# Performance work log

Hardware: AMD Instinct MI355X
Metric: run time of the kernel (lower is better)

Reference implementation:

```python
import jax, jax.numpy as jnp
import numpy as np

N_NODES = 50000
N_EDGES = 800000
D_IN = 128
D_OUT = 128
BN_EPS = 1e-5

# (component index, sign) per (column block j, row block i) of the octonion
# Hamilton matrix, matching make_octonion_mul's cat order exactly.
_OCT_TABLE = [
    [(0, 1), (1, -1), (2, -1), (3, -1), (4, -1), (5, -1), (6, -1), (7, -1)],
    [(1, 1), (0, 1), (3, -1), (2, 1), (5, -1), (4, 1), (7, 1), (6, -1)],
    [(2, 1), (3, 1), (0, 1), (1, -1), (6, -1), (7, -1), (4, 1), (5, 1)],
    [(3, 1), (2, -1), (1, 1), (0, 1), (7, -1), (6, 1), (5, -1), (4, 1)],
    [(4, 1), (5, 1), (6, 1), (7, 1), (0, 1), (1, -1), (2, -1), (3, -1)],
    [(5, 1), (4, -1), (7, 1), (6, -1), (1, 1), (0, 1), (3, 1), (2, -1)],
    [(6, 1), (7, -1), (4, -1), (5, 1), (2, 1), (3, -1), (0, 1), (1, 1)],
    [(7, 1), (6, 1), (5, -1), (4, -1), (3, 1), (2, 1), (1, -1), (0, 1)],
]


def make_octonion_mul(kernel):
    # kernel: [D_IN//8, D_OUT] -> hamilton: [D_IN, D_OUT]
    e = jnp.split(kernel, 8, axis=1)
    cols = [jnp.concatenate([s * e[i] for (i, s) in col], axis=0)
            for col in _OCT_TABLE]
    return jnp.concatenate(cols, axis=1)


def setup_inputs() -> dict:
    key = jax.random.key(0)
    k1, k2, k3, k4, k5 = jax.random.split(key, 5)
    stdv = np.sqrt(6.0 / (D_IN // 8 + D_OUT))
    return {
        "input": jax.random.normal(k1, (N_NODES, D_IN), dtype=jnp.float32),
        "adj_row": jax.random.randint(k2, (N_EDGES,), 0, N_NODES, dtype=jnp.int32),
        "adj_col": jax.random.randint(k3, (N_EDGES,), 0, N_NODES, dtype=jnp.int32),
        "adj_val": jax.random.uniform(k4, (N_EDGES,), dtype=jnp.float32),
        "weight": jax.random.uniform(k5, (D_IN // 8, D_OUT), dtype=jnp.float32,
                                     minval=-stdv, maxval=stdv),
        "gamma": jnp.ones((D_OUT,), dtype=jnp.float32),
        "beta": jnp.zeros((D_OUT,), dtype=jnp.float32),
    }


def reference(input, adj_row, adj_col, adj_val, weight, gamma, beta):
    hamilton = make_octonion_mul(weight)             # [D_IN, D_OUT]
    support = input @ hamilton                       # [N, D_OUT]
    # sparse adjacency spmm: out[r] += val * support[c]
    msg = adj_val[:, None] * support[adj_col]        # [E, D_OUT]
    out = jax.ops.segment_sum(msg, adj_row, num_segments=N_NODES)
    # BatchNorm1d (training mode: biased batch stats), then tanh
    mean = jnp.mean(out, axis=0)
    var = jnp.var(out, axis=0)
    normed = (out - mean) / jnp.sqrt(var + BN_EPS) * gamma + beta
    return jnp.tanh(normed)
```

## Files before the change

### kernel.cpp

```cpp
#include <hip/hip_runtime.h>
#include <hip/hip_fp16.h>
#include <math.h>

#define N_NODES 50000
#define N_EDGES 800000
#define D 128
#define BN_EPS 1e-5f
#define N_TILES 3125
#define CAP 48
#define SPMM_BLOCKS 2048
#define SCOLS 32
#define BINS 512
#define RPB 98
#define EPB 3125
#define SORTB 256
#define BCAP 2048
#define GEMMB 782

typedef __attribute__((ext_vector_type(8))) _Float16 half8;
typedef __attribute__((ext_vector_type(4))) float floatx4;

__device__ __constant__ int OCT_C[8][8] = {
    {0,1,2,3,4,5,6,7},
    {1,0,3,2,5,4,7,6},
    {2,3,0,1,6,7,4,5},
    {3,2,1,0,7,6,5,4},
    {4,5,6,7,0,1,2,3},
    {5,4,7,6,1,0,3,2},
    {6,7,4,5,2,3,0,1},
    {7,6,5,4,3,2,1,0}};
__device__ __constant__ float OCT_S[8][8] = {
    { 1,-1,-1,-1,-1,-1,-1,-1},
    { 1, 1,-1, 1,-1, 1, 1,-1},
    { 1, 1, 1,-1,-1,-1, 1, 1},
    { 1,-1, 1, 1,-1, 1,-1, 1},
    { 1, 1, 1, 1, 1,-1,-1,-1},
    { 1,-1, 1,-1, 1, 1, 1,-1},
    { 1,-1,-1, 1, 1,-1, 1, 1},
    { 1, 1,-1,-1, 1, 1,-1, 1}};

__global__ __launch_bounds__(256) void setup_kernel(const float* __restrict__ W,
                                                    __half* __restrict__ Ht,
                                                    float* __restrict__ stats,
                                                    int* __restrict__ bintail) {
    const int i = blockIdx.x * 256 + threadIdx.x;
    if (i < D * D) {
        int ccol = i >> 7, k = i & 127;
        int ii = k >> 4, kw = k & 15, j = ccol >> 4, m = ccol & 15;
        Ht[i] = __float2half(OCT_S[j][ii] * W[kw * D + OCT_C[j][ii] * 16 + m]);
    }
    if (i < 2 * D) stats[i] = 0.0f;
    if (i < BINS * 16) bintail[i] = 0;
}

__global__ __launch_bounds__(256) void sortgemm_kernel(const int* __restrict__ arow,
                                                       const int* __restrict__ acol,
                                                       const float* __restrict__ aval,
                                                       int* __restrict__ bintail,
                                                       uint2* __restrict__ binned,
                                                       const float* __restrict__ in,
                                                       const __half* __restrict__ Ht,
                                                       __half* __restrict__ support) {
    __shared__ uint2 stage[EPB];
    __shared__ int hist[BINS], pref[BINS], lbase[BINS], cursor[BINS];
    __shared__ int wtot[4];
    const int b = blockIdx.x;
    const int tid = threadIdx.x;
    if (b < SORTB) {
        const int lane = tid & 63, wid = tid >> 6;
        hist[tid] = 0; hist[tid + 256] = 0;
        __syncthreads();
        const int e0 = b * EPB, e1 = e0 + EPB;
        for (int i = e0 + tid; i < e1; i += 256)
            atomicAdd(&hist[arow[i] / RPB], 1);
        __syncthreads();
        int v0 = hist[2 * tid], v1 = hist[2 * tid + 1];
        int s = v0 + v1;
        int incl = s;
#pragma unroll
        for (int off = 1; off < 64; off <<= 1) {
            int t = __shfl_up(incl, off, 64);
            if (lane >= off) incl += t;
        }
        if (lane == 63) wtot[wid] = incl;
        __syncthreads();
        if (tid == 0) {
            int acc = 0;
#pragma unroll
            for (int w = 0; w < 4; ++w) { int t = wtot[w]; wtot[w] = acc; acc += t; }
        }
        __syncthreads();
        int excl = wtot[wid] + incl - s;
        pref[2 * tid] = excl;
        pref[2 * tid + 1] = excl + v0;
        cursor[2 * tid] = excl;
        cursor[2 * tid + 1] = excl + v0;
        lbase[2 * tid]     = v0 ? atomicAdd(&bintail[(2 * tid) * 16], v0) : 0;
        lbase[2 * tid + 1] = v1 ? atomicAdd(&bintail[(2 * tid + 1) * 16], v1) : 0;
        __syncthreads();
        for (int i = e0 + tid; i < e1; i += 256) {
            int r = arow[i];
            int bin = r / RPB;
            unsigned hv = (unsigned)__half_as_ushort(__float2half(aval[i]));
            unsigned pk = ((unsigned)acol[i] & 0xFFFFu) | (hv << 16);
            int pos = atomicAdd(&cursor[bin], 1);
            stage[pos] = make_uint2(pk, (unsigned)r);
        }
        __syncthreads();
        for (int j = tid; j < EPB; j += 256) {
            uint2 e = stage[j];
            int bin = (int)e.y / RPB;
            int gidx = lbase[bin] + (j - pref[bin]);
            if (gidx < BCAP) binned[(size_t)bin * BCAP + gidx] = e;
        }
        return;
    }
    const int wv = tid >> 6;
    const int tile = (b - SORTB) * 4 + wv;
    if (tile >= N_TILES) return;
    const int lane = tid & 63;
    const int s = lane & 15;
    const int t = lane >> 4;

    half8 bb[8][4];
#pragma unroll
    for (int kk = 0; kk < 4; ++kk)
#pragma unroll
        for (int n = 0; n < 8; ++n)
            bb[n][kk] = *reinterpret_cast<const half8*>(Ht + (size_t)(16 * n + s) * D + kk * 32 + 8 * t);

    const float* ap = in + (size_t)(tile * 16 + s) * D;
    half8 a[4];
#pragma unroll
    for (int kk = 0; kk < 4; ++kk) {
        float4 f0 = *reinterpret_cast<const float4*>(ap + kk * 32 + 8 * t);
        float4 f1 = *reinterpret_cast<const float4*>(ap + kk * 32 + 8 * t + 4);
        a[kk][0] = (_Float16)f0.x; a[kk][1] = (_Float16)f0.y;
        a[kk][2] = (_Float16)f0.z; a[kk][3] = (_Float16)f0.w;
        a[kk][4] = (_Float16)f1.x; a[kk][5] = (_Float16)f1.y;
        a[kk][6] = (_Float16)f1.z; a[kk][7] = (_Float16)f1.w;
    }

    floatx4 acc[8];
#pragma unroll
    for (int n = 0; n < 8; ++n) acc[n] = (floatx4){0.f, 0.f, 0.f, 0.f};
#pragma unroll
    for (int kk = 0; kk < 4; ++kk)
#pragma unroll
        for (int n = 0; n < 8; ++n)
            acc[n] = __builtin_amdgcn_mfma_f32_16x16x32_f16(a[kk], bb[n][kk], acc[n], 0, 0, 0);

    __half* sp = support + (size_t)(tile * 16 + 4 * t) * D + s;
#pragma unroll
    for (int r = 0; r < 4; ++r)
#pragma unroll
        for (int n = 0; n < 8; ++n)
            sp[(size_t)r * D + 16 * n] = __float2half(acc[n][r]);
}

__global__ __launch_bounds__(256) void spmm_kernel(const int* __restrict__ bintail,
                                                   const uint2* __restrict__ binned,
                                                   const __half* __restrict__ support,
                                                   __half* __restrict__ outh,
                                                   float* __restrict__ colsum,
                                                   float* __restrict__ colsq) {
    __shared__ unsigned lbucket[RPB * CAP];
    __shared__ int lcnt[RPB];
    __shared__ float lsum[SCOLS], lsq[SCOLS];

    const int tid = threadIdx.x;
    const int b = blockIdx.x;
    const int slice = (b & 7) >> 1;
    const int rank = ((b >> 3) << 1) | (b & 1);
    const int rbase = rank * RPB;

    if (tid < RPB) lcnt[tid] = 0;
    if (tid < SCOLS) { lsum[tid] = 0.f; lsq[tid] = 0.f; }
    for (int k = tid; k < RPB * CAP; k += 256) lbucket[k] = 0u;
    __syncthreads();
    int nb = bintail[rank * 16];
    nb = nb < BCAP ? nb : BCAP;
    const unsigned long long* seg = reinterpret_cast<const unsigned long long*>(
        binned + (size_t)rank * BCAP);
    for (int i = tid; i < nb; i += 256) {
        unsigned long long e = __builtin_nontemporal_load(seg + i);
        int rl = (int)(e >> 32) - rbase;
        int slot = atomicAdd(&lcnt[rl], 1);
        if (slot < CAP) lbucket[rl * CAP + slot] = (unsigned)e;
    }
    __syncthreads();

    const int lane = tid & 63;
    const int wv = tid >> 6;
    const int h = lane >> 4;
    const int cl = lane & 15;
    const int colbase = slice * SCOLS + cl * 2;
    const unsigned cb2 = (unsigned)(colbase * 2);
    const char* sbase = reinterpret_cast<const char*>(support);

    float s0 = 0.f, s1 = 0.f, q0 = 0.f, q1 = 0.f;

    for (int rl = wv * 2; rl < RPB; rl += 8) {
        const int row = rbase + rl;
        const int rowb = row + 1;
        int na = lcnt[rl]; na = na < CAP ? na : CAP;
        int nb2 = (rl + 1 < RPB) ? lcnt[rl + 1] : 0; nb2 = nb2 < CAP ? nb2 : CAP;
        const int nmax = na > nb2 ? na : nb2;
        __half2 acca = __half2half2(__ushort_as_half((unsigned short)0));
        __half2 accb = acca;

        {
            unsigned ua[8], ub[8];
            __half2 ga[8], gb[8];
#pragma unroll
            for (int j = 0; j < 8; ++j) {
                ua[j] = lbucket[rl * CAP + j * 4 + h];
                ub[j] = lbucket[(rl + 1 < RPB ? rl + 1 : rl) * CAP + j * 4 + h];
            }
            if (rl + 1 >= RPB) {
#pragma unroll
                for (int j = 0; j < 8; ++j) ub[j] = 0u;
            }
#pragma unroll
            for (int j = 0; j < 8; ++j) {
                ga[j] = *reinterpret_cast<const __half2*>(sbase + (((ua[j] & 0xFFFFu) << 8) + cb2));
                gb[j] = *reinterpret_cast<const __half2*>(sbase + (((ub[j] & 0xFFFFu) << 8) + cb2));
            }
#pragma unroll
            for (int j = 0; j < 8; ++j) {
                unsigned va2 = __builtin_amdgcn_perm(ua[j], ua[j], 0x07060706u);
                unsigned vb2 = __builtin_amdgcn_perm(ub[j], ub[j], 0x07060706u);
                acca = __hfma2(*reinterpret_cast<__half2*>(&va2), ga[j], acca);
                accb = __hfma2(*reinterpret_cast<__half2*>(&vb2), gb[j], accb);
            }
        }
        if (nmax > 32) {
            unsigned ua[4], ub[4];
            __half2 ga[4], gb[4];
#pragma unroll
            for (int j = 0; j < 4; ++j) {
                ua[j] = lbucket[rl * CAP + 32 + j * 4 + h];
                ub[j] = lbucket[(rl + 1 < RPB ? rl + 1 : rl) * CAP + 32 + j * 4 + h];
            }
            if (rl + 1 >= RPB) {
#pragma unroll
                for (int j = 0; j < 4; ++j) ub[j] = 0u;
            }
#pragma unroll
            for (int j = 0; j < 4; ++j) {
                ga[j] = *reinterpret_cast<const __half2*>(sbase + (((ua[j] & 0xFFFFu) << 8) + cb2));
                gb[j] = *reinterpret_cast<const __half2*>(sbase + (((ub[j] & 0xFFFFu) << 8) + cb2));
            }
#pragma unroll
            for (int j = 0; j < 4; ++j) {
                unsigned va2 = __builtin_amdgcn_perm(ua[j], ua[j], 0x07060706u);
                unsigned vb2 = __builtin_amdgcn_perm(ub[j], ub[j], 0x07060706u);
                acca = __hfma2(*reinterpret_cast<__half2*>(&va2), ga[j], acca);
                accb = __hfma2(*reinterpret_cast<__half2*>(&vb2), gb[j], accb);
            }
        }

#pragma unroll
        for (int off = 16; off <= 32; off <<= 1) {
            int ia = __shfl_xor(*reinterpret_cast<int*>(&acca), off);
            int ib = __shfl_xor(*reinterpret_cast<int*>(&accb), off);
            acca = __hadd2(acca, *reinterpret_cast<__half2*>(&ia));
            accb = __hadd2(accb, *reinterpret_cast<__half2*>(&ib));
        }
        if (h == 0) {
            if (row < N_NODES) {
                float2 fa = __half22float2(acca);
                __builtin_nontemporal_store(*reinterpret_cast<unsigned*>(&acca),
                    reinterpret_cast<unsigned*>(outh + (size_t)row * D + colbase));
                s0 += fa.x; s1 += fa.y; q0 += fa.x * fa.x; q1 += fa.y * fa.y;
            }
            if (rowb < N_NODES && rl + 1 < RPB) {
                float2 fb = __half22float2(accb);
                __builtin_nontemporal_store(*reinterpret_cast<unsigned*>(&accb),
                    reinterpret_cast<unsigned*>(outh + (size_t)rowb * D + colbase));
                s0 += fb.x; s1 += fb.y; q0 += fb.x * fb.x; q1 += fb.y * fb.y;
            }
        }
    }

    if (h == 0) {
        atomicAdd(&lsum[cl * 2 + 0], s0); atomicAdd(&lsum[cl * 2 + 1], s1);
        atomicAdd(&lsq[cl * 2 + 0], q0);  atomicAdd(&lsq[cl * 2 + 1], q1);
    }
    __syncthreads();
    if (tid < SCOLS) {
        atomicAdd(&colsum[slice * SCOLS + tid], lsum[tid]);
        atomicAdd(&colsq[slice * SCOLS + tid], lsq[tid]);
    }
}

__global__ __launch_bounds__(256) void bn_tanh_kernel(const __half* __restrict__ outh,
                                                      float* __restrict__ out,
                                                      const float* __restrict__ colsum,
                                                      const float* __restrict__ colsq,
                                                      const float* __restrict__ gamma,
                                                      const float* __restrict__ beta) {
    __shared__ float scale[D], shift[D];
    const int tid = threadIdx.x;
    if (tid < D) {
        float mean = colsum[tid] * (1.0f / N_NODES);
        float var  = colsq[tid] * (1.0f / N_NODES) - mean * mean;
        float sc   = rsqrtf(var + BN_EPS) * gamma[tid];
        scale[tid] = sc;
        shift[tid] = beta[tid] - mean * sc;
    }
    __syncthreads();
    const int nq = N_NODES * D / 8;
    floatx4* outv = reinterpret_cast<floatx4*>(out);
    for (int i = blockIdx.x * 256 + tid; i < nq; i += gridDim.x * 256) {
        uint4 v = reinterpret_cast<const uint4*>(outh)[i];
        const int c = (i & 15) * 8;
        float r[8];
        float2 f;
        f = __half22float2(*reinterpret_cast<__half2*>(&v.x)); r[0] = f.x; r[1] = f.y;
        f = __half22float2(*reinterpret_cast<__half2*>(&v.y)); r[2] = f.x; r[3] = f.y;
        f = __half22float2(*reinterpret_cast<__half2*>(&v.z)); r[4] = f.x; r[5] = f.y;
        f = __half22float2(*reinterpret_cast<__half2*>(&v.w)); r[6] = f.x; r[7] = f.y;
#pragma unroll
        for (int k = 0; k < 8; ++k) {
            float x = r[k] * scale[c + k] + shift[c + k];
            float e = __expf(2.0f * x);
            r[k] = 1.0f - 2.0f / (1.0f + e);
        }
        floatx4 o0 = {r[0], r[1], r[2], r[3]};
        floatx4 o1 = {r[4], r[5], r[6], r[7]};
        __builtin_nontemporal_store(o0, outv + i * 2 + 0);
        __builtin_nontemporal_store(o1, outv + i * 2 + 1);
    }
}

extern "C" void kernel_launch(void* const* d_in, const int* in_sizes, int n_in,
                              void* d_out, int out_size, void* d_ws, size_t ws_size,
                              hipStream_t stream) {
    const float* input  = (const float*)d_in[0];
    const int*   arow   = (const int*)d_in[1];
    const int*   acol   = (const int*)d_in[2];
    const float* aval   = (const float*)d_in[3];
    const float* weight = (const float*)d_in[4];
    const float* gamma  = (const float*)d_in[5];
    const float* beta   = (const float*)d_in[6];
    float* out = (float*)d_out;

    __half*   support = (__half*)d_ws;
    __half*   outh    = (__half*)(support + (size_t)N_NODES * D);
    uint2*    binned  = (uint2*)(outh + (size_t)N_NODES * D);
    float*    colsum  = (float*)(binned + (size_t)BINS * BCAP);
    float*    colsq   = colsum + D;
    int*      bintail = (int*)(colsum + 2 * D);
    __half*   Ht      = (__half*)(bintail + BINS * 16);

    setup_kernel<<<64, 256, 0, stream>>>(weight, Ht, colsum, bintail);
    sortgemm_kernel<<<SORTB + GEMMB, 256, 0, stream>>>(arow, acol, aval, bintail, binned,
                                                       input, Ht, support);
    spmm_kernel<<<SPMM_BLOCKS, 256, 0, stream>>>(bintail, binned, support, outh,
                                                 colsum, colsq);
    bn_tanh_kernel<<<2048, 256, 0, stream>>>(outh, out, colsum, colsq, gamma, beta);
}
```

Measured before the change: 86.23 us.

## Widen SpMM column slice to 64 and halve block count

Each SpMM block now covers 64 columns instead of 32, so every lane gathers 4 half values (8 bytes) per edge with a uint2 load and keeps two half2 accumulators per row. The grid drops from 2048 to 1024 blocks, so each row bucket's edge list is binned into shared memory by 2 blocks instead of 4. The aim is less redundant bucket-building work and wider gather loads. In exchange there are fewer blocks to hide gather latency and more registers per thread.

After: 87.79 us. About the same (+1.8%).

```diff
diff --git a/kernel.cpp b/kernel.cpp
--- a/kernel.cpp
+++ b/kernel.cpp
@@ -8,8 +8,8 @@
 #define BN_EPS 1e-5f
 #define N_TILES 3125
 #define CAP 48
-#define SPMM_BLOCKS 2048
-#define SCOLS 32
+#define SPMM_BLOCKS 1024
+#define SCOLS 64
 #define BINS 512
 #define RPB 98
 #define EPB 3125
@@ -170,8 +170,8 @@
 
     const int tid = threadIdx.x;
     const int b = blockIdx.x;
-    const int slice = (b & 7) >> 1;
-    const int rank = ((b >> 3) << 1) | (b & 1);
+    const int slice = (b & 7) >> 2;
+    const int rank = ((b >> 3) << 2) | (b & 3);
     const int rbase = rank * RPB;
 
     if (tid < RPB) lcnt[tid] = 0;
@@ -194,11 +194,12 @@
     const int wv = tid >> 6;
     const int h = lane >> 4;
     const int cl = lane & 15;
-    const int colbase = slice * SCOLS + cl * 2;
+    const int colbase = slice * SCOLS + cl * 4;
     const unsigned cb2 = (unsigned)(colbase * 2);
     const char* sbase = reinterpret_cast<const char*>(support);
 
-    float s0 = 0.f, s1 = 0.f, q0 = 0.f, q1 = 0.f;
+    float s0 = 0.f, s1 = 0.f, s2 = 0.f, s3 = 0.f;
+    float q0 = 0.f, q1 = 0.f, q2 = 0.f, q3 = 0.f;
 
     for (int rl = wv * 2; rl < RPB; rl += 8) {
         const int row = rbase + rl;
@@ -206,86 +207,103 @@
         int na = lcnt[rl]; na = na < CAP ? na : CAP;
         int nb2 = (rl + 1 < RPB) ? lcnt[rl + 1] : 0; nb2 = nb2 < CAP ? nb2 : CAP;
         const int nmax = na > nb2 ? na : nb2;
-        __half2 acca = __half2half2(__ushort_as_half((unsigned short)0));
-        __half2 accb = acca;
+        __half2 acca0 = __half2half2(__ushort_as_half((unsigned short)0));
+        __half2 acca1 = acca0, accb0 = acca0, accb1 = acca0;
+        const int rl1 = (rl + 1 < RPB) ? rl + 1 : rl;
+        const bool hasb = (rl + 1 < RPB);
 
         {
             unsigned ua[8], ub[8];
-            __half2 ga[8], gb[8];
+            uint2 ga[8], gb[8];
 #pragma unroll
             for (int j = 0; j < 8; ++j) {
                 ua[j] = lbucket[rl * CAP + j * 4 + h];
-                ub[j] = lbucket[(rl + 1 < RPB ? rl + 1 : rl) * CAP + j * 4 + h];
-            }
-            if (rl + 1 >= RPB) {
-#pragma unroll
-                for (int j = 0; j < 8; ++j) ub[j] = 0u;
+                ub[j] = hasb ? lbucket[rl1 * CAP + j * 4 + h] : 0u;
             }
 #pragma unroll
             for (int j = 0; j < 8; ++j) {
-                ga[j] = *reinterpret_cast<const __half2*>(sbase + (((ua[j] & 0xFFFFu) << 8) + cb2));
-                gb[j] = *reinterpret_cast<const __half2*>(sbase + (((ub[j] & 0xFFFFu) << 8) + cb2));
+                ga[j] = *reinterpret_cast<const uint2*>(sbase + (((ua[j] & 0xFFFFu) << 8) + cb2));
+                gb[j] = *reinterpret_cast<const uint2*>(sbase + (((ub[j] & 0xFFFFu) << 8) + cb2));
             }
 #pragma unroll
             for (int j = 0; j < 8; ++j) {
                 unsigned va2 = __builtin_amdgcn_perm(ua[j], ua[j], 0x07060706u);
                 unsigned vb2 = __builtin_amdgcn_perm(ub[j], ub[j], 0x07060706u);
-                acca = __hfma2(*reinterpret_cast<__half2*>(&va2), ga[j], acca);
-                accb = __hfma2(*reinterpret_cast<__half2*>(&vb2), gb[j], accb);
+                __half2 va = *reinterpret_cast<__half2*>(&va2);
+                __half2 vb = *reinterpret_cast<__half2*>(&vb2);
+                acca0 = __hfma2(va, *reinterpret_cast<__half2*>(&ga[j].x), acca0);
+                acca1 = __hfma2(va, *reinterpret_cast<__half2*>(&ga[j].y), acca1);
+                accb0 = __hfma2(vb, *reinterpret_cast<__half2*>(&gb[j].x), accb0);
+                accb1 = __hfma2(vb, *reinterpret_cast<__half2*>(&gb[j].y), accb1);
             }
         }
         if (nmax > 32) {
             unsigned ua[4], ub[4];
-            __half2 ga[4], gb[4];
+            uint2 ga[4], gb[4];
 #pragma unroll
             for (int j = 0; j < 4; ++j) {
                 ua[j] = lbucket[rl * CAP + 32 + j * 4 + h];
-                ub[j] = lbucket[(rl + 1 < RPB ? rl + 1 : rl) * CAP + 32 + j * 4 + h];
-            }
-            if (rl + 1 >= RPB) {
-#pragma unroll
-                for (int j = 0; j < 4; ++j) ub[j] = 0u;
+                ub[j] = hasb ? lbucket[rl1 * CAP + 32 + j * 4 + h] : 0u;
             }
 #pragma unroll
             for (int j = 0; j < 4; ++j) {
-                ga[j] = *reinterpret_cast<const __half2*>(sbase + (((ua[j] & 0xFFFFu) << 8) + cb2));
-                gb[j] = *reinterpret_cast<const __half2*>(sbase + (((ub[j] & 0xFFFFu) << 8) + cb2));
+                ga[j] = *reinterpret_cast<const uint2*>(sbase + (((ua[j] & 0xFFFFu) << 8) + cb2));
+                gb[j] = *reinterpret_cast<const uint2*>(sbase + (((ub[j] & 0xFFFFu) << 8) + cb2));
             }
 #pragma unroll
             for (int j = 0; j < 4; ++j) {
                 unsigned va2 = __builtin_amdgcn_perm(ua[j], ua[j], 0x07060706u);
                 unsigned vb2 = __builtin_amdgcn_perm(ub[j], ub[j], 0x07060706u);
-                acca = __hfma2(*reinterpret_cast<__half2*>(&va2), ga[j], acca);
-                accb = __hfma2(*reinterpret_cast<__half2*>(&vb2), gb[j], accb);
+                __half2 va = *reinterpret_cast<__half2*>(&va2);
+                __half2 vb = *reinterpret_cast<__half2*>(&vb2);
+                acca0 = __hfma2(va, *reinterpret_cast<__half2*>(&ga[j].x), acca0);
+                acca1 = __hfma2(va, *reinterpret_cast<__half2*>(&ga[j].y), acca1);
+                accb0 = __hfma2(vb, *reinterpret_cast<__half2*>(&gb[j].x), accb0);
+                accb1 = __hfma2(vb, *reinterpret_cast<__half2*>(&gb[j].y), accb1);
             }
         }
 
 #pragma unroll
         for (int off = 16; off <= 32; off <<= 1) {
-            int ia = __shfl_xor(*reinterpret_cast<int*>(&acca), off);
-            int ib = __shfl_xor(*reinterpret_cast<int*>(&accb), off);
-            acca = __hadd2(acca, *reinterpret_cast<__half2*>(&ia));
-            accb = __hadd2(accb, *reinterpret_cast<__half2*>(&ib));
+            int i0 = __shfl_xor(*reinterpret_cast<int*>(&acca0), off);
+            int i1 = __shfl_xor(*reinterpret_cast<int*>(&acca1), off);
+            int i2 = __shfl_xor(*reinterpret_cast<int*>(&accb0), off);
+            int i3 = __shfl_xor(*reinterpret_cast<int*>(&accb1), off);
+            acca0 = __hadd2(acca0, *reinterpret_cast<__half2*>(&i0));
+            acca1 = __hadd2(acca1, *reinterpret_cast<__half2*>(&i1));
+            accb0 = __hadd2(accb0, *reinterpret_cast<__half2*>(&i2));
+            accb1 = __hadd2(accb1, *reinterpret_cast<__half2*>(&i3));
         }
         if (h == 0) {
             if (row < N_NODES) {
-                float2 fa = __half22float2(acca);
-                __builtin_nontemporal_store(*reinterpret_cast<unsigned*>(&acca),
-                    reinterpret_cast<unsigned*>(outh + (size_t)row * D + colbase));
-                s0 += fa.x; s1 += fa.y; q0 += fa.x * fa.x; q1 += fa.y * fa.y;
-            }
-            if (rowb < N_NODES && rl + 1 < RPB) {
-                float2 fb = __half22float2(accb);
-                __builtin_nontemporal_store(*reinterpret_cast<unsigned*>(&accb),
+                float2 f0 = __half22float2(acca0);
+                float2 f1 = __half22float2(acca1);
+                uint2 pk;
+                pk.x = *reinterpret_cast<unsigned*>(&acca0);
+                pk.y = *reinterpret_cast<unsigned*>(&acca1);
+                __builtin_nontemporal_store(pk.x, reinterpret_cast<unsigned*>(outh + (size_t)row * D + colbase));
+                __builtin_nontemporal_store(pk.y, reinterpret_cast<unsigned*>(outh + (size_t)row * D + colbase + 2));
+                s0 += f0.x; s1 += f0.y; s2 += f1.x; s3 += f1.y;
+                q0 += f0.x * f0.x; q1 += f0.y * f0.y; q2 += f1.x * f1.x; q3 += f1.y * f1.y;
+            }
+            if (rowb < N_NODES && hasb) {
+                float2 f0 = __half22float2(accb0);
+                float2 f1 = __half22float2(accb1);
+                __builtin_nontemporal_store(*reinterpret_cast<unsigned*>(&accb0),
                     reinterpret_cast<unsigned*>(outh + (size_t)rowb * D + colbase));
-                s0 += fb.x; s1 += fb.y; q0 += fb.x * fb.x; q1 += fb.y * fb.y;
+                __builtin_nontemporal_store(*reinterpret_cast<unsigned*>(&accb1),
+                    reinterpret_cast<unsigned*>(outh + (size_t)rowb * D + colbase + 2));
+                s0 += f0.x; s1 += f0.y; s2 += f1.x; s3 += f1.y;
+                q0 += f0.x * f0.x; q1 += f0.y * f0.y; q2 += f1.x * f1.x; q3 += f1.y * f1.y;
             }
         }
     }
 
     if (h == 0) {
-        atomicAdd(&lsum[cl * 2 + 0], s0); atomicAdd(&lsum[cl * 2 + 1], s1);
-        atomicAdd(&lsq[cl * 2 + 0], q0);  atomicAdd(&lsq[cl * 2 + 1], q1);
+        atomicAdd(&lsum[cl * 4 + 0], s0); atomicAdd(&lsum[cl * 4 + 1], s1);
+        atomicAdd(&lsum[cl * 4 + 2], s2); atomicAdd(&lsum[cl * 4 + 3], s3);
+        atomicAdd(&lsq[cl * 4 + 0], q0);  atomicAdd(&lsq[cl * 4 + 1], q1);
+        atomicAdd(&lsq[cl * 4 + 2], q2);  atomicAdd(&lsq[cl * 4 + 3], q3);
     }
     __syncthreads();
     if (tid < SCOLS) {
```
